# Kernel optimization log

Hardware: AMD Instinct MI355X
Metric: run time of the kernel (lower is better)

The kernel has to match this reference:

```python
import jax, jax.numpy as jnp
import numpy as np

B, S, H, V, L = 8, 1024, 1024, 512, 6
NEG_INF = -10000000.0  # matches torch neg_inf constant


def setup_inputs() -> dict:
    key = jax.random.key(0)
    ks = jax.random.split(key, 13)
    s = 0.02
    return {
        "inputs": jax.random.randint(ks[0], (B, S), 0, V),
        "embedding": jax.random.normal(ks[1], (V, H), jnp.float32) * s,
        "Wq": jax.random.normal(ks[2], (L, H, H), jnp.float32) * s,
        "bq": jnp.zeros((L, H), jnp.float32),
        "Wk": jax.random.normal(ks[3], (L, H, H), jnp.float32) * s,
        "bk": jnp.zeros((L, H), jnp.float32),
        "Wv": jax.random.normal(ks[4], (L, H, H), jnp.float32) * s,
        "bv": jnp.zeros((L, H), jnp.float32),
        "Wm": jax.random.normal(ks[5], (L, H, H), jnp.float32) * s,
        "bm": jnp.zeros((L, H), jnp.float32),
        "Wout": jax.random.normal(ks[6], (H, V), jnp.float32) * s,
        "bout": jnp.zeros((V,), jnp.float32),
    }


def reference(inputs, embedding, Wq, bq, Wk, bk, Wv, bv, Wm, bm, Wout, bout):
    Hd = embedding.shape[1]
    seq = inputs.shape[1]
    scale = jax.lax.rsqrt(jnp.asarray(Hd, jnp.float32))
    idx = jnp.arange(seq)
    # mask[key, query]: additive NEG_INF where key > query (strict lower triangle)
    mask = jnp.where(idx[:, None] > idx[None, :], jnp.float32(NEG_INF), jnp.float32(0.0))
    x = embedding[inputs]  # [B, S, H]
    n_layers = Wq.shape[0]
    attns = []
    for l in range(n_layers):
        q = x @ Wq[l] + bq[l]
        k = x @ Wk[l] + bk[l]
        v = x @ Wv[l] + bv[l]
        # [B, key, query], softmax over key axis (dim=1), exactly as original
        logits = jnp.einsum('bkh,bqh->bkq', k, q) * scale + mask
        attn = jax.nn.softmax(logits, axis=1)
        ctx = jnp.einsum('bkq,bkh->bqh', attn, v)  # attn^T @ v
        residual = x + ctx
        x = residual + jax.nn.relu(ctx @ Wm[l] + bm[l])
        attns.append(attn)
    out = x @ Wout + bout  # [B, S, V]
    return out, jnp.stack(attns)  # attns: [L, B, S, S]
```

## Files before the change

kernel.cpp:

```cpp
#include <hip/hip_runtime.h>
#include <stdint.h>

typedef unsigned short u16;
typedef unsigned int u32;
typedef __bf16 bf16x8 __attribute__((ext_vector_type(8)));
typedef float floatx4 __attribute__((ext_vector_type(4)));

#define NEG_INF_F (-10000000.0f)
#define MFMA16 __builtin_amdgcn_mfma_f32_16x16x32_bf16

__device__ __forceinline__ float bf2f(u16 u) {
    union { u32 u; float f; } x; x.u = ((u32)u) << 16; return x.f;
}
__device__ __forceinline__ u16 f2bf(float f) {
    union { float f; u32 u; } x; x.f = f;
    u32 r = x.u + 0x7fffu + ((x.u >> 16) & 1u);
    return (u16)(r >> 16);
}

__device__ __forceinline__ void async_cp16(const void* g, void* l) {
    __builtin_amdgcn_global_load_lds(
        (const __attribute__((address_space(1))) void*)g,
        (__attribute__((address_space(3))) void*)l, 16, 0, 0);
}

enum { EPI_QKV = 0, EPI_LOGITS = 1, EPI_CTX = 2, EPI_MLP = 3, EPI_OUT = 4 };

template <int EPI>
__global__ __launch_bounds__(256) void gemm_bt(
    const u16* __restrict__ A, int lda, long long aBatch,
    const u16* __restrict__ B, int ldb, long long bBatch,
    void* __restrict__ Cv, int ldc, long long cBatch,
    int K,
    const float* __restrict__ bias,
    const u16* __restrict__ ctxb,
    u16* __restrict__ xb,
    float scale, int nx, int ny)
{
    __shared__ __align__(16) u16 sA[128 * 64];
    __shared__ __align__(16) u16 sB[128 * 64];

    const int tid  = threadIdx.x;
    const int wave = tid >> 6;
    const int lane = tid & 63;

    int bxE, byE, bz;
    if constexpr (EPI == EPI_LOGITS) {
        bz = blockIdx.x & 7;
        int t = blockIdx.x >> 3;
        int tq = (int)((sqrtf(8.0f * t + 1.0f) - 1.0f) * 0.5f);
        while ((tq + 1) * (tq + 2) / 2 <= t) ++tq;
        while (tq * (tq + 1) / 2 > t) --tq;
        bxE = tq;
        byE = t - tq * (tq + 1) / 2;
    } else if constexpr (EPI == EPI_CTX) {
        bz = blockIdx.x & 7;
        int t = blockIdx.x >> 3;
        bxE = t & 7;
        byE = t >> 3;
    } else {
        bz = 0;
        const int k = blockIdx.x & 7, r = blockIdx.x >> 3;
        if (nx >= 8) { const int xp = nx >> 3; bxE = xp * k + (r % xp); byE = r / xp; }
        else         { bxE = k >> 1; byE = (k & 1) * (ny >> 1) + r; }
    }
    int Keff = K;
    if constexpr (EPI == EPI_CTX) Keff = min(K, (byE + 1) * 128);

    const u16* Ab = A + (long long)bz * aBatch + (long long)(byE * 128) * lda;
    const u16* Bb = B + (long long)bz * bBatch + (long long)(bxE * 128) * ldb;

    const int wm = wave >> 1, wn = wave & 1;
    const int quad = lane >> 4;

    const int srowoff = lane >> 3;
    const int gf      = (lane & 7) ^ ((lane >> 3) & 7);

    const int ra = 64 * wm + (lane & 15);
    const int rb = 64 * wn + (lane & 15);
    const int rx7 = lane & 7;

    floatx4 zero = {0.f, 0.f, 0.f, 0.f};
    floatx4 acc[4][4];
#pragma unroll
    for (int i = 0; i < 4; ++i)
#pragma unroll
        for (int j = 0; j < 4; ++j) acc[i][j] = zero;

    for (int k0 = 0; k0 < Keff; k0 += 64) {
#pragma unroll
        for (int i = 0; i < 4; ++i) {
            const int c = wave * 4 + i;
            const int r = c * 8 + srowoff;
            async_cp16(Ab + (long long)r * lda + k0 + gf * 8, &sA[c * 512 + lane * 8]);
            async_cp16(Bb + (long long)r * ldb + k0 + gf * 8, &sB[c * 512 + lane * 8]);
        }
        __syncthreads();

#pragma unroll
        for (int kk = 0; kk < 64; kk += 32) {
            const int gbase = kk >> 3;
            const int ga = ((gbase + quad) ^ rx7) << 3;
            bf16x8 af[4], bf[4];
#pragma unroll
            for (int mi = 0; mi < 4; ++mi)
                af[mi] = *(const bf16x8*)&sA[(ra + 16 * mi) * 64 + ga];
#pragma unroll
            for (int ni = 0; ni < 4; ++ni)
                bf[ni] = *(const bf16x8*)&sB[(rb + 16 * ni) * 64 + ga];
#pragma unroll
            for (int mi = 0; mi < 4; ++mi)
#pragma unroll
                for (int ni = 0; ni < 4; ++ni)
                    acc[mi][ni] = MFMA16(af[mi], bf[ni], acc[mi][ni], 0, 0, 0);
        }
        __syncthreads();
    }

    const int m0 = byE * 128 + 64 * wm + (quad << 2);
    const int n0 = bxE * 128 + 64 * wn + (lane & 15);
#pragma unroll
    for (int mi = 0; mi < 4; ++mi) {
#pragma unroll
        for (int ni = 0; ni < 4; ++ni) {
            const int gn = n0 + ni * 16;
#pragma unroll
            for (int r = 0; r < 4; ++r) {
                const int gm = m0 + mi * 16 + r;
                float v = acc[mi][ni][r];
                if constexpr (EPI == EPI_QKV) {
                    v += bias[gn];
                    ((u16*)Cv)[(long long)gm * ldc + gn] = f2bf(v);
                } else if constexpr (EPI == EPI_LOGITS) {
                    v = v * scale + (gm > gn ? NEG_INF_F : 0.0f);
                    ((float*)Cv)[(long long)bz * cBatch + (long long)gm * ldc + gn] = v;
                } else if constexpr (EPI == EPI_CTX) {
                    ((u16*)Cv)[(long long)bz * cBatch + (long long)gm * ldc + gn] = f2bf(v);
                } else if constexpr (EPI == EPI_MLP) {
                    const long long idx = (long long)gm * ldc + gn;
                    v += bias[gn];
                    v = fmaxf(v, 0.0f);
                    float xv = bf2f(xb[idx]) + bf2f(ctxb[idx]) + v;
                    xb[idx] = f2bf(xv);
                } else {
                    v += bias[gn];
                    ((float*)Cv)[(long long)gm * ldc + gn] = v;
                }
            }
        }
    }
}

template <int EPI>
__global__ __launch_bounds__(512, 2) void gemm3s(
    const u16* __restrict__ A, int lda,
    const u16* __restrict__ Bw, int ldb,
    void* __restrict__ Cv, int ldc,
    int K, const float* __restrict__ bias,
    const u16* __restrict__ ctxb, u16* __restrict__ xb)
{
    __shared__ __align__(16) u16 sA[3][256 * 64];
    __shared__ __align__(16) u16 sB[3][128 * 64];

    const int tid  = threadIdx.x;
    const int wave = tid >> 6;
    const int lane = tid & 63;
    const int wm   = wave >> 1, wn = wave & 1;
    const int quad = lane >> 4;

    const int k8 = blockIdx.x & 7;
    const int r  = blockIdx.x >> 3;
    const int bxE = r >> 2;
    const int byE = k8 * 4 + (r & 3);

    const u16* Ab = A  + (long long)(byE * 256) * lda;
    const u16* Bb = Bw + (long long)(bxE * 128) * ldb;

    const int srow = tid >> 3;
    const int gf   = (tid & 7) ^ ((tid >> 3) & 7);
    const long long aSrc = (long long)srow * lda + gf * 8;
    const long long bSrc = (long long)srow * ldb + gf * 8;
    const int dst = (wave << 9) + lane * 8;

#define STA(nb, c, k0) async_cp16(Ab + (long long)((c) * 64) * lda + (k0) + aSrc, \
                                  &sA[nb][(c) * 4096 + dst])
#define STB(nb, c, k0) async_cp16(Bb + (long long)((c) * 64) * ldb + (k0) + bSrc, \
                                  &sB[nb][(c) * 4096 + dst])

    const int ra  = wm * 64 + (lane & 15);
    const int rb  = wn * 64 + (lane & 15);
    const int rx7 = lane & 7;

    floatx4 zero = {0.f, 0.f, 0.f, 0.f};
    floatx4 acc[4][4];
#pragma unroll
    for (int i = 0; i < 4; ++i)
#pragma unroll
        for (int j = 0; j < 4; ++j) acc[i][j] = zero;

    const int NT = K >> 6;

    STA(0, 0, 0);  STA(0, 1, 0);  STA(0, 2, 0);  STA(0, 3, 0);
    STB(0, 0, 0);  STB(0, 1, 0);
    STA(1, 0, 64); STA(1, 1, 64); STA(1, 2, 64); STA(1, 3, 64);
    STB(1, 0, 64); STB(1, 1, 64);

    int cb = 0;
#pragma unroll 3
    for (int t = 0; t < NT; ++t) {
        if (t + 1 < NT) asm volatile("s_waitcnt vmcnt(6)" ::: "memory");
        else            asm volatile("s_waitcnt vmcnt(0)" ::: "memory");
        __builtin_amdgcn_s_barrier();

        const int  nb = (cb == 0) ? 2 : cb - 1;
        const int  kn = (t + 2) << 6;
        const bool st = (t + 2) < NT;
        const u16* pA = &sA[cb][0];
        const u16* pB = &sB[cb][0];

        bf16x8 af[4], bf0, bf1;

        if (st) { STA(nb, 0, kn); STA(nb, 1, kn); }
        {
            const int g = (quad ^ rx7) << 3;
#pragma unroll
            for (int mi = 0; mi < 4; ++mi)
                af[mi] = *(const bf16x8*)&pA[(ra + 16 * mi) * 64 + g];
            bf0 = *(const bf16x8*)&pB[rb * 64 + g];
            bf1 = *(const bf16x8*)&pB[(rb + 16) * 64 + g];
        }
        __builtin_amdgcn_s_setprio(1);
#pragma unroll
        for (int mi = 0; mi < 4; ++mi) {
            acc[mi][0] = MFMA16(af[mi], bf0, acc[mi][0], 0, 0, 0);
            acc[mi][1] = MFMA16(af[mi], bf1, acc[mi][1], 0, 0, 0);
        }
        __builtin_amdgcn_s_setprio(0);

        if (st) { STA(nb, 2, kn); STA(nb, 3, kn); }
        {
            const int g = (quad ^ rx7) << 3;
            bf0 = *(const bf16x8*)&pB[(rb + 32) * 64 + g];
            bf1 = *(const bf16x8*)&pB[(rb + 48) * 64 + g];
        }
        __builtin_amdgcn_s_setprio(1);
#pragma unroll
        for (int mi = 0; mi < 4; ++mi) {
            acc[mi][2] = MFMA16(af[mi], bf0, acc[mi][2], 0, 0, 0);
            acc[mi][3] = MFMA16(af[mi], bf1, acc[mi][3], 0, 0, 0);
        }
        __builtin_amdgcn_s_setprio(0);

        if (st) { STB(nb, 0, kn); }
        {
            const int g = ((4 + quad) ^ rx7) << 3;
#pragma unroll
            for (int mi = 0; mi < 4; ++mi)
                af[mi] = *(const bf16x8*)&pA[(ra + 16 * mi) * 64 + g];
            bf0 = *(const bf16x8*)&pB[rb * 64 + g];
            bf1 = *(const bf16x8*)&pB[(rb + 16) * 64 + g];
        }
        __builtin_amdgcn_s_setprio(1);
#pragma unroll
        for (int mi = 0; mi < 4; ++mi) {
            acc[mi][0] = MFMA16(af[mi], bf0, acc[mi][0], 0, 0, 0);
            acc[mi][1] = MFMA16(af[mi], bf1, acc[mi][1], 0, 0, 0);
        }
        __builtin_amdgcn_s_setprio(0);

        if (st) { STB(nb, 1, kn); }
        {
            const int g = ((4 + quad) ^ rx7) << 3;
            bf0 = *(const bf16x8*)&pB[(rb + 32) * 64 + g];
            bf1 = *(const bf16x8*)&pB[(rb + 48) * 64 + g];
        }
        __builtin_amdgcn_s_setprio(1);
#pragma unroll
        for (int mi = 0; mi < 4; ++mi) {
            acc[mi][2] = MFMA16(af[mi], bf0, acc[mi][2], 0, 0, 0);
            acc[mi][3] = MFMA16(af[mi], bf1, acc[mi][3], 0, 0, 0);
        }
        __builtin_amdgcn_s_setprio(0);

        cb = (cb == 2) ? 0 : cb + 1;
    }
#undef STA
#undef STB

    const int m0 = byE * 256 + wm * 64 + (quad << 2);
    const int n0 = bxE * 128 + wn * 64 + (lane & 15);
#pragma unroll
    for (int mi = 0; mi < 4; ++mi) {
#pragma unroll
        for (int ni = 0; ni < 4; ++ni) {
            const int gn = n0 + ni * 16;
            const float bb = bias[gn];
#pragma unroll
            for (int rr = 0; rr < 4; ++rr) {
                const int gm = m0 + mi * 16 + rr;
                float v = acc[mi][ni][rr] + bb;
                if constexpr (EPI == EPI_QKV) {
                    ((u16*)Cv)[(long long)gm * ldc + gn] = f2bf(v);
                } else {
                    const long long idx = (long long)gm * ldc + gn;
                    v = fmaxf(v, 0.0f);
                    float xv = bf2f(xb[idx]) + bf2f(ctxb[idx]) + v;
                    xb[idx] = f2bf(xv);
                }
            }
        }
    }
}

template <int L, int H, int V>
__global__ void setup_weights(const float* __restrict__ Wq, const float* __restrict__ Wk,
                              const float* __restrict__ Wv, const float* __restrict__ Wm,
                              const float* __restrict__ Wout,
                              const float* __restrict__ bq, const float* __restrict__ bk,
                              const float* __restrict__ bv,
                              u16* __restrict__ WqkvT, u16* __restrict__ WmT,
                              u16* __restrict__ WoutT, float* __restrict__ bqkv)
{
    const int z = blockIdx.z;
    if (z == 4 * L + 1) {
        int i = ((blockIdx.y * 16 + blockIdx.x) * 256) + threadIdx.y * 64 + threadIdx.x;
        if (i < L * 3 * H) {
            int l = i / (3 * H), j = i % (3 * H);
            float v = (j < H) ? bq[l * H + j]
                    : (j < 2 * H) ? bk[l * H + j - H]
                                  : bv[l * H + j - 2 * H];
            bqkv[i] = v;
        }
        return;
    }

    const float* in;
    u16* outp;
    int inStride, outStride;
    if (z == 4 * L) {
        if (blockIdx.x >= V / 64) return;
        in = Wout; inStride = V;
        outp = WoutT; outStride = H;
    } else {
        const int which = z / L, l = z % L;
        inStride = H; outStride = H;
        if (which == 3) { in = Wm + (long long)l * H * H; outp = WmT + (long long)l * H * H; }
        else {
            in   = (which == 0 ? Wq : which == 1 ? Wk : Wv) + (long long)l * H * H;
            outp = WqkvT + (long long)l * 3 * H * H + (long long)which * H * H;
        }
    }

    __shared__ float tile[64][65];
    const int r0 = blockIdx.y * 64, c0 = blockIdx.x * 64;
    const int x = threadIdx.x, y = threadIdx.y;
#pragma unroll
    for (int j = 0; j < 16; ++j) {
        int r = y + j * 4;
        tile[r][x] = in[(long long)(r0 + r) * inStride + c0 + x];
    }
    __syncthreads();
#pragma unroll
    for (int j = 0; j < 16; ++j) {
        int r = y + j * 4;
        outp[(long long)(c0 + r) * outStride + r0 + x] = f2bf(tile[x][r]);
    }
}

__global__ __launch_bounds__(1024) void attn_post(
    float* __restrict__ attn, long long aStride,
    u16* __restrict__ attnT, long long tStride,
    const u16* __restrict__ qkv, u16* __restrict__ Vt)
{
    const int zone = blockIdx.y;
    if (zone < 8) {
        __shared__ float sm[64][16], sl[64][16], sm2[8][16], sl2[8][16];
        __shared__ float sM[16], sInv[16];

        float* base = attn + (long long)zone * aStride;
        const int x = threadIdx.x, ky = threadIdx.y;
        const int q = blockIdx.x * 16 + x;

        float v[16];
        float m = -3.4e38f, l = 0.f;
#pragma unroll
        for (int j = 0; j < 16; ++j) {
            const int k = ky * 16 + j;
            float vj = NEG_INF_F;
            if (k <= q) vj = base[(long long)k * 1024 + q];
            v[j] = vj;
            float mn = fmaxf(m, vj);
            l = l * __expf(m - mn) + __expf(vj - mn);
            m = mn;
        }
        sm[ky][x] = m;
        sl[ky][x] = l;
        __syncthreads();
        if (ky < 8) {
            float M = -3.4e38f, L = 0.f;
#pragma unroll
            for (int t = 0; t < 8; ++t) {
                float mm = sm[ky + 8 * t][x], ll = sl[ky + 8 * t][x];
                float mn = fmaxf(M, mm);
                L = L * __expf(M - mn) + ll * __expf(mm - mn);
                M = mn;
            }
            sm2[ky][x] = M;
            sl2[ky][x] = L;
        }
        __syncthreads();
        if (ky == 0) {
            float M = -3.4e38f, L = 0.f;
#pragma unroll
            for (int t = 0; t < 8; ++t) {
                float mm = sm2[t][x], ll = sl2[t][x];
                float mn = fmaxf(M, mm);
                L = L * __expf(M - mn) + ll * __expf(mm - mn);
                M = mn;
            }
            sM[x]   = M;
            sInv[x] = 1.0f / L;
        }
        __syncthreads();
        const float M = sM[x], inv = sInv[x];

        u16 pb[16];
#pragma unroll
        for (int j = 0; j < 16; ++j) {
            float p = __expf(v[j] - M) * inv;
            base[(long long)(ky * 16 + j) * 1024 + q] = p;
            pb[j] = f2bf(p);
        }
        u16* trow = attnT + (long long)zone * tStride + (long long)q * 1024 + ky * 16;
        ((uint4*)trow)[0] = *(const uint4*)&pb[0];
        ((uint4*)trow)[1] = *(const uint4*)&pb[8];
    } else {
        const int b = zone - 8;
        const u16* Vb = qkv + 2 * 1024 + (long long)b * (1024LL * 3072);
        u16* Ob       = Vt + (long long)b * (1024LL * 1024);
        __shared__ float tile[64][65];
        const int tid = threadIdx.y * 16 + threadIdx.x;
        const int tx = tid & 63, ty = tid >> 6;
#pragma unroll
        for (int rep = 0; rep < 4; ++rep) {
            const int T = blockIdx.x + rep * 64;
            const int s0 = (T >> 4) * 64, h0 = (T & 15) * 64;
            __syncthreads();
#pragma unroll
            for (int j = 0; j < 4; ++j) {
                const int s = j * 16 + ty;
                tile[s][tx] = bf2f(Vb[(long long)(s0 + s) * 3072 + h0 + tx]);
            }
            __syncthreads();
#pragma unroll
            for (int j = 0; j < 4; ++j) {
                const int h = j * 16 + ty;
                Ob[(long long)(h0 + h) * 1024 + s0 + tx] = f2bf(tile[tx][h]);
            }
        }
    }
}

__global__ void embed_kernel(const int* __restrict__ tok, const float* __restrict__ emb,
                             u16* __restrict__ xb)
{
    const int row = blockIdx.x;
    const int t   = tok[row];
    float4 v = ((const float4*)(emb + (long long)t * 1024))[threadIdx.x];
    uint2 p;
    p.x = (u32)f2bf(v.x) | ((u32)f2bf(v.y) << 16);
    p.y = (u32)f2bf(v.z) | ((u32)f2bf(v.w) << 16);
    ((uint2*)(xb + (long long)row * 1024))[threadIdx.x] = p;
}

extern "C" void kernel_launch(void* const* d_in, const int* in_sizes, int n_in,
                              void* d_out, int out_size, void* d_ws, size_t ws_size,
                              hipStream_t stream)
{
    const int*   tok  = (const int*)d_in[0];
    const float* emb  = (const float*)d_in[1];
    const float* Wq   = (const float*)d_in[2];
    const float* bq   = (const float*)d_in[3];
    const float* Wk   = (const float*)d_in[4];
    const float* bk   = (const float*)d_in[5];
    const float* Wv   = (const float*)d_in[6];
    const float* bv   = (const float*)d_in[7];
    const float* Wm   = (const float*)d_in[8];
    const float* bm   = (const float*)d_in[9];
    const float* Wout = (const float*)d_in[10];
    const float* bout = (const float*)d_in[11];
    float* out = (float*)d_out;

    constexpr int B = 8, S = 1024, H = 1024, V = 512, L = 6;
    constexpr long long M = (long long)B * S;

    char* ws = (char*)d_ws;
    u16*   WqkvT = (u16*)ws;   ws += (long long)L * 3 * H * H * 2;
    u16*   WmT   = (u16*)ws;   ws += (long long)L * H * H * 2;
    u16*   WoutT = (u16*)ws;   ws += (long long)V * H * 2;
    float* bqkv  = (float*)ws; ws += (long long)L * 3 * H * 4;
    u16*   xb    = (u16*)ws;   ws += M * H * 2;
    u16*   QKV   = (u16*)ws;   ws += M * 3 * H * 2;
    u16*   attnT = (u16*)ws;   ws += (long long)B * S * S * 2;
    u16*   Vt    = (u16*)ws;   ws += (long long)B * S * S * 2;
    u16*   ctxb  = (u16*)ws;   ws += M * H * 2;

    float* attnOut = out + (long long)B * S * V;

    setup_weights<L, H, V><<<dim3(16, 16, 4 * L + 2), dim3(64, 4), 0, stream>>>(
        Wq, Wk, Wv, Wm, Wout, bq, bk, bv, WqkvT, WmT, WoutT, bqkv);
    embed_kernel<<<M, 256, 0, stream>>>(tok, emb, xb);

    for (int l = 0; l < L; ++l) {
        gemm3s<EPI_QKV><<<768, 512, 0, stream>>>(
            xb, H, WqkvT + (long long)l * 3 * H * H, H,
            QKV, 3 * H, H, bqkv + l * 3 * H, nullptr, nullptr);

        float* attnL = attnOut + (long long)l * B * S * S;
        gemm_bt<EPI_LOGITS><<<288, 256, 0, stream>>>(
            QKV + H, 3 * H, (long long)S * 3 * H,
            QKV, 3 * H, (long long)S * 3 * H,
            attnL, S, (long long)S * S, H,
            nullptr, nullptr, nullptr, 0.03125f, 0, 0);

        attn_post<<<dim3(64, 16), dim3(16, 64), 0, stream>>>(
            attnL, (long long)S * S, attnT, (long long)S * S, QKV, Vt);

        gemm_bt<EPI_CTX><<<512, 256, 0, stream>>>(
            attnT, S, (long long)S * S, Vt, S, (long long)S * S,
            ctxb, H, (long long)S * H, S,
            nullptr, nullptr, nullptr, 0.f, 0, 0);

        gemm3s<EPI_MLP><<<256, 512, 0, stream>>>(
            ctxb, H, WmT + (long long)l * H * H, H,
            nullptr, H, H, bm + l * H, ctxb, xb);
    }

    gemm_bt<EPI_OUT><<<256, 256, 0, stream>>>(
        xb, H, 0, WoutT, H, 0, out, V, 0, H,
        bout, nullptr, nullptr, 0.f, 4, 64);
}
```

Baseline: 1.546 ms.

## Restructure 3-stage GEMM main loop with ping-pong barriers and route MLP GEMM to gemm_bt

The triple-buffered GEMM loop is reorganised. Each k-tile now loads all A fragments and half the B fragments up front, and the async global-to-LDS copies are regrouped into two batches fenced by extra barriers and an lgkmcnt wait. The vmcnt wait moves to the end of the iteration, which aims to overlap memory traffic with MFMA clusters in a ping-pong style. Separately, the MLP projection switches from the 256x128 tile kernel to the smaller-tile gemm_bt kernel with 512 blocks, which adds more barriers per iteration but may fill the GPU better.

```diff
diff --git a/kernel.cpp b/kernel.cpp
--- a/kernel.cpp
+++ b/kernel.cpp
@@ -152,7 +152,7 @@
 }
 
 template <int EPI>
-__global__ __launch_bounds__(512, 2) void gemm3s(
+__global__ __launch_bounds__(512, 2) void gemm3p(
     const u16* __restrict__ A, int lda,
     const u16* __restrict__ Bw, int ldb,
     void* __restrict__ Cv, int ldc,
@@ -167,6 +167,7 @@
     const int lane = tid & 63;
     const int wm   = wave >> 1, wn = wave & 1;
     const int quad = lane >> 4;
+    const int rx7  = lane & 7;
 
     const int k8 = blockIdx.x & 7;
     const int r  = blockIdx.x >> 3;
@@ -187,9 +188,8 @@
 #define STB(nb, c, k0) async_cp16(Bb + (long long)((c) * 64) * ldb + (k0) + bSrc, \
                                   &sB[nb][(c) * 4096 + dst])
 
-    const int ra  = wm * 64 + (lane & 15);
-    const int rb  = wn * 64 + (lane & 15);
-    const int rx7 = lane & 7;
+    const int ra = wm * 64 + (lane & 15);
+    const int rb = wn * 64 + (lane & 15);
 
     floatx4 zero = {0.f, 0.f, 0.f, 0.f};
     floatx4 acc[4][4];
@@ -204,83 +204,63 @@
     STB(0, 0, 0);  STB(0, 1, 0);
     STA(1, 0, 64); STA(1, 1, 64); STA(1, 2, 64); STA(1, 3, 64);
     STB(1, 0, 64); STB(1, 1, 64);
+    asm volatile("s_waitcnt vmcnt(6)" ::: "memory");
+    __builtin_amdgcn_s_barrier();
 
     int cb = 0;
-#pragma unroll 3
     for (int t = 0; t < NT; ++t) {
-        if (t + 1 < NT) asm volatile("s_waitcnt vmcnt(6)" ::: "memory");
-        else            asm volatile("s_waitcnt vmcnt(0)" ::: "memory");
-        __builtin_amdgcn_s_barrier();
-
         const int  nb = (cb == 0) ? 2 : cb - 1;
         const int  kn = (t + 2) << 6;
         const bool st = (t + 2) < NT;
-        const u16* pA = &sA[cb][0];
-        const u16* pB = &sB[cb][0];
-
-        bf16x8 af[4], bf0, bf1;
-
-        if (st) { STA(nb, 0, kn); STA(nb, 1, kn); }
-        {
-            const int g = (quad ^ rx7) << 3;
+
+        bf16x8 aF[2][4], bF[2][2];
+
+#pragma unroll
+        for (int h = 0; h < 2; ++h) {
+            const int g = (((h << 2) + quad) ^ rx7) << 3;
 #pragma unroll
             for (int mi = 0; mi < 4; ++mi)
-                af[mi] = *(const bf16x8*)&pA[(ra + 16 * mi) * 64 + g];
-            bf0 = *(const bf16x8*)&pB[rb * 64 + g];
-            bf1 = *(const bf16x8*)&pB[(rb + 16) * 64 + g];
-        }
+                aF[h][mi] = *(const bf16x8*)&sA[cb][(ra + 16 * mi) * 64 + g];
+#pragma unroll
+            for (int ni = 0; ni < 2; ++ni)
+                bF[h][ni] = *(const bf16x8*)&sB[cb][(rb + 16 * ni) * 64 + g];
+        }
+        if (st) { STA(nb, 0, kn); STA(nb, 1, kn); STA(nb, 2, kn); }
+        __builtin_amdgcn_s_barrier();
+        asm volatile("s_waitcnt lgkmcnt(0)" ::: "memory");
         __builtin_amdgcn_s_setprio(1);
 #pragma unroll
-        for (int mi = 0; mi < 4; ++mi) {
-            acc[mi][0] = MFMA16(af[mi], bf0, acc[mi][0], 0, 0, 0);
-            acc[mi][1] = MFMA16(af[mi], bf1, acc[mi][1], 0, 0, 0);
-        }
+        for (int h = 0; h < 2; ++h)
+#pragma unroll
+            for (int mi = 0; mi < 4; ++mi)
+#pragma unroll
+                for (int ni = 0; ni < 2; ++ni)
+                    acc[mi][ni] = MFMA16(aF[h][mi], bF[h][ni], acc[mi][ni], 0, 0, 0);
         __builtin_amdgcn_s_setprio(0);
-
-        if (st) { STA(nb, 2, kn); STA(nb, 3, kn); }
-        {
-            const int g = (quad ^ rx7) << 3;
-            bf0 = *(const bf16x8*)&pB[(rb + 32) * 64 + g];
-            bf1 = *(const bf16x8*)&pB[(rb + 48) * 64 + g];
-        }
+        __builtin_amdgcn_s_barrier();
+
+        bf16x8 bG[2][2];
+#pragma unroll
+        for (int h = 0; h < 2; ++h) {
+            const int g = (((h << 2) + quad) ^ rx7) << 3;
+#pragma unroll
+            for (int ni = 0; ni < 2; ++ni)
+                bG[h][ni] = *(const bf16x8*)&sB[cb][(rb + 32 + 16 * ni) * 64 + g];
+        }
+        if (st) { STA(nb, 3, kn); STB(nb, 0, kn); STB(nb, 1, kn); }
+        __builtin_amdgcn_s_barrier();
+        asm volatile("s_waitcnt lgkmcnt(0)" ::: "memory");
         __builtin_amdgcn_s_setprio(1);
 #pragma unroll
-        for (int mi = 0; mi < 4; ++mi) {
-            acc[mi][2] = MFMA16(af[mi], bf0, acc[mi][2], 0, 0, 0);
-            acc[mi][3] = MFMA16(af[mi], bf1, acc[mi][3], 0, 0, 0);
-        }
+        for (int h = 0; h < 2; ++h)
+#pragma unroll
+            for (int mi = 0; mi < 4; ++mi)
+#pragma unroll
+                for (int ni = 0; ni < 2; ++ni)
+                    acc[mi][2 + ni] = MFMA16(aF[h][mi], bG[h][ni], acc[mi][2 + ni], 0, 0, 0);
         __builtin_amdgcn_s_setprio(0);
-
-        if (st) { STB(nb, 0, kn); }
-        {
-            const int g = ((4 + quad) ^ rx7) << 3;
-#pragma unroll
-            for (int mi = 0; mi < 4; ++mi)
-                af[mi] = *(const bf16x8*)&pA[(ra + 16 * mi) * 64 + g];
-            bf0 = *(const bf16x8*)&pB[rb * 64 + g];
-            bf1 = *(const bf16x8*)&pB[(rb + 16) * 64 + g];
-        }
-        __builtin_amdgcn_s_setprio(1);
-#pragma unroll
-        for (int mi = 0; mi < 4; ++mi) {
-            acc[mi][0] = MFMA16(af[mi], bf0, acc[mi][0], 0, 0, 0);
-            acc[mi][1] = MFMA16(af[mi], bf1, acc[mi][1], 0, 0, 0);
-        }
-        __builtin_amdgcn_s_setprio(0);
-
-        if (st) { STB(nb, 1, kn); }
-        {
-            const int g = ((4 + quad) ^ rx7) << 3;
-            bf0 = *(const bf16x8*)&pB[(rb + 32) * 64 + g];
-            bf1 = *(const bf16x8*)&pB[(rb + 48) * 64 + g];
-        }
-        __builtin_amdgcn_s_setprio(1);
-#pragma unroll
-        for (int mi = 0; mi < 4; ++mi) {
-            acc[mi][2] = MFMA16(af[mi], bf0, acc[mi][2], 0, 0, 0);
-            acc[mi][3] = MFMA16(af[mi], bf1, acc[mi][3], 0, 0, 0);
-        }
-        __builtin_amdgcn_s_setprio(0);
+        asm volatile("s_waitcnt vmcnt(6)" ::: "memory");
+        __builtin_amdgcn_s_barrier();
 
         cb = (cb == 2) ? 0 : cb + 1;
     }
@@ -512,7 +492,7 @@
     embed_kernel<<<M, 256, 0, stream>>>(tok, emb, xb);
 
     for (int l = 0; l < L; ++l) {
-        gemm3s<EPI_QKV><<<768, 512, 0, stream>>>(
+        gemm3p<EPI_QKV><<<768, 512, 0, stream>>>(
             xb, H, WqkvT + (long long)l * 3 * H * H, H,
             QKV, 3 * H, H, bqkv + l * 3 * H, nullptr, nullptr);
 
@@ -531,9 +511,9 @@
             ctxb, H, (long long)S * H, S,
             nullptr, nullptr, nullptr, 0.f, 0, 0);
 
-        gemm3s<EPI_MLP><<<256, 512, 0, stream>>>(
-            ctxb, H, WmT + (long long)l * H * H, H,
-            nullptr, H, H, bm + l * H, ctxb, xb);
+        gemm_bt<EPI_MLP><<<512, 256, 0, stream>>>(
+            ctxb, H, 0, WmT + (long long)l * H * H, H, 0,
+            nullptr, H, 0, H, bm + l * H, ctxb, xb, 0.f, 8, 64);
     }
 
     gemm_bt<EPI_OUT><<<256, 256, 0, stream>>>(
```

New measurement: 1.356 ms. -12.3%, faster.
